# Performance work log

Measured on AMD Instinct MI355X. Metric: run time of the kernel, lower is better.

Reference implementation:

```python
import jax, jax.numpy as jnp
import numpy as np

N, DIM, H, D = 8192, 1152, 16, 72
SEGS = 4  # equal-length image segments


def setup_inputs() -> dict:
    key = jax.random.key(0)
    ks = jax.random.split(key, 8)
    s = 0.02
    return {
        "hidden_states": jax.random.normal(ks[0], (N, DIM), jnp.float32),
        "cos": jax.random.uniform(ks[1], (N, D), jnp.float32, -1.0, 1.0),
        "sin": jax.random.uniform(ks[2], (N, D), jnp.float32, -1.0, 1.0),
        "cu_seqlens": (jnp.arange(SEGS + 1, dtype=jnp.int32) * (N // SEGS)),
        "w_qkv": jax.random.normal(ks[3], (DIM, 3 * DIM), jnp.float32) * s,
        "b_qkv": jax.random.normal(ks[4], (3 * DIM,), jnp.float32) * s,
        "w_proj": jax.random.normal(ks[5], (DIM, DIM), jnp.float32) * s,
        "b_proj": jax.random.normal(ks[6], (DIM,), jnp.float32) * s,
    }


def _rope(x, cos, sin):
    # x: [N, H, D]; cos/sin: [N, 1, D]
    half = x.shape[-1] // 2
    x1, x2 = x[..., :half], x[..., half:]
    rot = jnp.concatenate([-x2, x1], axis=-1)
    return x * cos + rot * sin


def reference(hidden_states, cos, sin, cu_seqlens, w_qkv, b_qkv, w_proj, b_proj):
    n = hidden_states.shape[0]
    qkv = (hidden_states @ w_qkv + b_qkv).reshape(n, 3, H, D)
    q, k, v = qkv[:, 0], qkv[:, 1], qkv[:, 2]
    c = cos[:, None, :]
    s = sin[:, None, :]
    q = _rope(q, c, s)
    k = _rope(k, c, s)
    # equal-length segments derived statically from cu_seqlens
    segs = int(cu_seqlens.shape[0]) - 1
    L = n // segs
    qs = q.reshape(segs, L, H, D)
    ks = k.reshape(segs, L, H, D)
    vs = v.reshape(segs, L, H, D)
    scale = D ** -0.5
    scores = jnp.einsum("slhd,smhd->shlm", qs, ks) * scale
    attn = jax.nn.softmax(scores, axis=-1)
    out = jnp.einsum("shlm,smhd->slhd", attn, vs).reshape(n, DIM)
    return out @ w_proj + b_proj
```

## Files before the change

### kernel.cpp

```cpp
#include <hip/hip_runtime.h>
#include <hip/hip_bf16.h>
#include <cstdint>
#include <cstddef>

typedef __bf16 bf16;
typedef __attribute__((ext_vector_type(4))) __bf16 bf16x4;
typedef __attribute__((ext_vector_type(8))) __bf16 bf16x8;
typedef __attribute__((ext_vector_type(4))) float f32x4;
typedef __attribute__((ext_vector_type(16))) float f32x16;
typedef __attribute__((ext_vector_type(4))) float floatx4;
typedef __attribute__((ext_vector_type(2))) unsigned uint2_t;
typedef __attribute__((ext_vector_type(4))) unsigned uint4_t;

#define NTOK 8192
#define DIMM 1152
#define NH   16
#define HD   72
#define SEGS 4
#define SEGL 2048

__device__ __forceinline__ void gload16(const void* gsrc, void* ldst) {
  __builtin_amdgcn_global_load_lds(
      (const __attribute__((address_space(1))) void*)gsrc,
      (__attribute__((address_space(3))) void*)ldst,
      16, 0, 0);
}

__device__ __forceinline__ unsigned cvtpk(float a, float b) {
  unsigned r;
  asm volatile("v_cvt_pk_bf16_f32 %0, %1, %2" : "=v"(r) : "v"(a), "v"(b));
  return r;
}

__global__ __launch_bounds__(256) void k_prep(const float* __restrict__ hs,
                                              bf16* __restrict__ hsb,
                                              const float* __restrict__ wq,
                                              bf16* __restrict__ wqT,
                                              const float* __restrict__ wp,
                                              bf16* __restrict__ wpT) {
  __shared__ bf16 tile[64][73];
  const int b = blockIdx.x, t = threadIdx.x;
  if (b < 4608) {
    int i = b * 256 + t;
    const floatx4* s = (const floatx4*)hs + (size_t)i * 2;
    floatx4 a = s[0], c = s[1];
    uint4_t o;
    o[0] = cvtpk(a.x, a.y);
    o[1] = cvtpk(a.z, a.w);
    o[2] = cvtpk(c.x, c.y);
    o[3] = cvtpk(c.z, c.w);
    *((uint4_t*)hsb + i) = o;
    return;
  }
  const float* src; bf16* dst; int R, C, bx, by;
  if (b < 4608 + 1008) {
    int idx = b - 4608;
    src = wq; dst = wqT; R = 1152; C = 3456; bx = idx % 56; by = idx / 56;
  } else {
    int idx = b - 5616;
    src = wp; dst = wpT; R = 1152; C = 1152; bx = idx % 18; by = idx / 18;
  }
  int bc = bx * 64, br = by * 64;
#pragma unroll
  for (int i = 0; i < 16; i++) {
    int idx = i * 256 + t;
    int r = idx >> 6, c = idx & 63;
    float v = (bc + c < C) ? src[(size_t)(br + r) * C + bc + c] : 0.f;
    tile[c][r] = (bf16)v;
  }
  __syncthreads();
#pragma unroll
  for (int i = 0; i < 16; i++) {
    int idx = i * 256 + t;
    int r = idx >> 6, c = idx & 63;
    dst[(size_t)(bc + r) * R + br + c] = tile[r][c];
  }
}

template <int BM, int BN, int MI, int NI, int THREADS, bool OUT_F32, int MW>
__global__ __launch_bounds__(THREADS, MW) void k_gemmP(const bf16* __restrict__ A,
                                                       const bf16* __restrict__ Bt,
                                                       const float* __restrict__ bias,
                                                       void* __restrict__ Cout,
                                                       int M, int Nreal, int K, int gx) {
  __shared__ bf16 sA[3][BM * 32];
  __shared__ bf16 sB[3][BN * 32];
  constexpr int WN = BN / (NI * 16);
  constexpr int nA = (BM * 4) / THREADS;
  constexpr int nB = (BN * 4) / THREADS;
  constexpr int NLD = nA + nB;
  static_assert(NLD == 3 || NLD == 4 || NLD == 6, "vmcnt literal");
  const int t = threadIdx.x, wave = t >> 6, lane = t & 63;
  const int lr = lane & 15, lg = lane >> 4;
  const int nwg = gridDim.x, bid = blockIdx.x;
  const int swz = (bid & 7) * (nwg >> 3) + (bid >> 3);
  const int bx = swz % gx, by = swz / gx;
  const int m0 = by * BM, n0 = bx * BN;
  const int wr = wave / WN, wc = wave % WN;
  const int NS = K >> 5;

  f32x4 acc[MI][NI];
#pragma unroll
  for (int i = 0; i < MI; i++)
#pragma unroll
    for (int j = 0; j < NI; j++)
#pragma unroll
      for (int q = 0; q < 4; q++) acc[i][j][q] = 0.f;

  const bf16* Ab = A + (size_t)m0 * K;
  const bf16* Bb = Bt + (size_t)n0 * K;
  const int glsw = ((t & 3) ^ ((t >> 3) & 3)) * 8;
  const int rbase = t >> 2;

  auto STAGE = [&](int slot, int k0) {
#pragma unroll
    for (int p = 0; p < nA; ++p)
      gload16(Ab + (size_t)(rbase + p * (THREADS / 4)) * K + k0 + glsw,
              (char*)&sA[slot][0] + p * (THREADS * 16) + wave * 1024);
#pragma unroll
    for (int p = 0; p < nB; ++p)
      gload16(Bb + (size_t)(rbase + p * (THREADS / 4)) * K + k0 + glsw,
              (char*)&sB[slot][0] + p * (THREADS * 16) + wave * 1024);
  };

  const int swz4 = (lr >> 1) & 3;
  const int aoff = (wr * MI * 16 + lr) * 32 + ((lg ^ swz4) * 8);
  const int boff = (wc * NI * 16 + lr) * 32 + ((lg ^ swz4) * 8);

  STAGE(0, 0);
  STAGE(1, 32);

  int slot = 0;
  for (int j = 0; j < NS; ++j) {
    if (j == NS - 1) {
      asm volatile("s_waitcnt vmcnt(0)" ::: "memory");
    } else if constexpr (NLD == 3) {
      asm volatile("s_waitcnt vmcnt(3)" ::: "memory");
    } else if constexpr (NLD == 4) {
      asm volatile("s_waitcnt vmcnt(4)" ::: "memory");
    } else {
      asm volatile("s_waitcnt vmcnt(6)" ::: "memory");
    }
    __builtin_amdgcn_s_barrier();
    __builtin_amdgcn_sched_barrier(0);
    bf16x8 av[MI], bv[NI];
#pragma unroll
    for (int mi = 0; mi < MI; mi++)
      av[mi] = *(const bf16x8*)&sA[slot][aoff + mi * 512];
#pragma unroll
    for (int ni = 0; ni < NI; ni++)
      bv[ni] = *(const bf16x8*)&sB[slot][boff + ni * 512];
    asm volatile("s_waitcnt lgkmcnt(0)" ::: "memory");
    __builtin_amdgcn_sched_barrier(0);
    if (j + 2 < NS) {
      int s2 = slot + 2; if (s2 >= 3) s2 -= 3;
      STAGE(s2, (j + 2) * 32);
    }
    __builtin_amdgcn_s_setprio(1);
#pragma unroll
    for (int mi = 0; mi < MI; mi++)
#pragma unroll
      for (int ni = 0; ni < NI; ni++)
        acc[mi][ni] = __builtin_amdgcn_mfma_f32_16x16x32_bf16(av[mi], bv[ni], acc[mi][ni], 0, 0, 0);
    __builtin_amdgcn_s_setprio(0);
    if (++slot == 3) slot = 0;
  }

#pragma unroll
  for (int mi = 0; mi < MI; ++mi)
#pragma unroll
    for (int ni = 0; ni < NI; ++ni) {
      int col = n0 + wc * NI * 16 + ni * 16 + lr;
      if (col < Nreal) {
        float bc_ = bias[col];
#pragma unroll
        for (int j = 0; j < 4; j++) {
          int row = m0 + wr * MI * 16 + mi * 16 + lg * 4 + j;
          float v = acc[mi][ni][j] + bc_;
          if (OUT_F32)
            ((float*)Cout)[(size_t)row * Nreal + col] = v;
          else
            ((bf16*)Cout)[(size_t)row * Nreal + col] = (bf16)v;
        }
      }
    }
}

__global__ __launch_bounds__(256) void k_ropev(const bf16* __restrict__ qkv,
                                               const float* __restrict__ cs,
                                               const float* __restrict__ sn,
                                               bf16* __restrict__ Qp,
                                               bf16* __restrict__ Kp,
                                               bf16* __restrict__ Vt) {
  __shared__ bf16 tl[64][80];
  const int bid = blockIdx.x, t = threadIdx.x;
  if (bid < 2048) {
    const float QS = 0.17002323f;
    const int n0 = bid * 4;
#pragma unroll
    for (int it = 0; it < 6; ++it) {
      int idx = it * 256 + t;
      int tok = idx / 384;
      int r = idx - tok * 384;
      int which = r / 192;
      int r2 = r - which * 192;
      int h = r2 / 12;
      int d0 = (r2 - h * 12) * 8;
      int n = n0 + tok;
      bf16* dst = which ? Kp : Qp;
      size_t ob = ((((size_t)((n >> 11) * NH + h)) * 3 + (d0 >> 5)) * SEGL +
                   (n & 2047)) * 32 + (d0 & 31);
      if (d0 >= HD) {
        uint4_t z = {0u, 0u, 0u, 0u};
        *(uint4_t*)&dst[ob] = z;
        continue;
      }
      const bf16* rowp = qkv + (size_t)n * (3 * DIMM) + which * DIMM + h * HD;
      bf16x8 xv = *(const bf16x8*)&rowp[d0];
      float ov[8];
      if (d0 == 32) {
        bf16x4 a = *(const bf16x4*)&rowp[68];
        bf16x4 b = *(const bf16x4*)&rowp[0];
#pragma unroll
        for (int j = 0; j < 4; j++) { ov[j] = -(float)a[j]; ov[j + 4] = (float)b[j]; }
      } else if (d0 < 32) {
        bf16x4 a = *(const bf16x4*)&rowp[d0 + 36];
        bf16x4 b = *(const bf16x4*)&rowp[d0 + 40];
#pragma unroll
        for (int j = 0; j < 4; j++) { ov[j] = -(float)a[j]; ov[j + 4] = -(float)b[j]; }
      } else {
        bf16x4 a = *(const bf16x4*)&rowp[d0 - 36];
        bf16x4 b = *(const bf16x4*)&rowp[d0 - 32];
#pragma unroll
        for (int j = 0; j < 4; j++) { ov[j] = (float)a[j]; ov[j + 4] = (float)b[j]; }
      }
      const float* cr = cs + (size_t)n * HD + d0;
      const float* sr = sn + (size_t)n * HD + d0;
      floatx4 c0 = *(const floatx4*)cr, c1 = *(const floatx4*)(cr + 4);
      floatx4 s0 = *(const floatx4*)sr, s1 = *(const floatx4*)(sr + 4);
      float vv[8];
#pragma unroll
      for (int j = 0; j < 4; j++) {
        vv[j] = (float)xv[j] * c0[j] + ov[j] * s0[j];
        vv[j + 4] = (float)xv[j + 4] * c1[j] + ov[j + 4] * s1[j];
      }
      if (!which) {
#pragma unroll
        for (int j = 0; j < 8; j++) vv[j] *= QS;
      }
      uint4_t w;
      w[0] = cvtpk(vv[0], vv[1]);
      w[1] = cvtpk(vv[2], vv[3]);
      w[2] = cvtpk(vv[4], vv[5]);
      w[3] = cvtpk(vv[6], vv[7]);
      *(uint4_t*)&dst[ob] = w;
    }
  } else {
    int idx2 = bid - 2048;
    int s = idx2 >> 9, h = (idx2 >> 5) & 15, l0 = (idx2 & 31) * 64;
    for (int idx = t; idx < 64 * HD; idx += 256) {
      int l = idx / HD, d = idx - l * HD;
      tl[l][d] = qkv[(size_t)(s * SEGL + l0 + l) * (3 * DIMM) + 2 * DIMM + h * HD + d];
    }
    __syncthreads();
    for (int idx = t; idx < 96 * 64; idx += 256) {
      int d = idx >> 6, l = idx & 63;
      bf16 v = (d < HD) ? tl[l][d] : ((d == HD) ? (bf16)1.f : (bf16)0.f);
      Vt[((size_t)(s * NH + h) * 96 + d) * SEGL + l0 + l] = v;
    }
  }
}

__global__ __launch_bounds__(256, 2) void k_attn(const bf16* __restrict__ Qg,
                                                 const bf16* __restrict__ Kg,
                                                 const bf16* __restrict__ Vg,
                                                 bf16* __restrict__ Oo) {
  __shared__ bf16 sK[2][3 * 64 * 32];
  __shared__ bf16 sV[2][96 * 64];
  const int t = threadIdx.x, wave = t >> 6, lane = t & 63;
  const int c = lane & 31, hi = lane >> 5;
  const int bid = blockIdx.x;
  const int g = ((bid >> 6) << 3) | (bid & 7);
  const int qt = (bid >> 3) & 7;
  const int s = g >> 4, h = g & 15, q0 = qt * 256;
  const bf16* Qb = Qg + (size_t)(s * NH + h) * 3 * SEGL * 32;
  const bf16* Kb = Kg + (size_t)(s * NH + h) * 3 * SEGL * 32;
  const bf16* Vb = Vg + (size_t)(s * NH + h) * 96 * SEGL;

  const bf16* kq[3];
  const bf16* vq[3];
#pragma unroll
  for (int i = 0; i < 3; i++) {
    int ch = wave * 3 + i;
    int kk = ch >> 2;
    int r = (ch & 3) * 16 + (lane >> 2);
    int gg = (lane & 3) ^ ((r >> 1) & 3);
    kq[i] = Kb + (size_t)kk * (SEGL * 32) + (size_t)r * 32 + gg * 8;
    int rv = ch * 8 + (lane >> 3);
    int gv = (lane & 7) ^ (rv & 7);
    vq[i] = Vb + (size_t)rv * SEGL + gv * 8;
  }

  bf16x8 Qf[2][5];
#pragma unroll
  for (int sni = 0; sni < 2; sni++)
#pragma unroll
    for (int kk = 0; kk < 5; kk++) {
      int qr = q0 + wave * 64 + sni * 32 + c;
      Qf[sni][kk] = *(const bf16x8*)&Qb[(size_t)(kk >> 1) * (SEGL * 32) +
                                        (size_t)qr * 32 + ((kk & 1) * 2 + hi) * 8];
    }

#pragma unroll
  for (int i = 0; i < 3; i++) {
    gload16(kq[i], (char*)sK[0] + (wave * 3 + i) * 1024);
    gload16(vq[i], (char*)sV[0] + (wave * 3 + i) * 1024);
    kq[i] += 2048;
    vq[i] += 64;
  }
  __syncthreads();

  f32x16 accO[3][2];
#pragma unroll
  for (int df = 0; df < 3; df++)
#pragma unroll
    for (int sni = 0; sni < 2; sni++)
#pragma unroll
      for (int r = 0; r < 16; r++) accO[df][sni][r] = 0.f;
  f32x16 ZC;
#pragma unroll
  for (int r = 0; r < 16; r++) ZC[r] = 0.f;

  int cur = 0;
  for (int tile = 0; tile < 32; ++tile) {
    if (tile + 1 < 32) {
#pragma unroll
      for (int i = 0; i < 3; i++) {
        gload16(kq[i], (char*)sK[cur ^ 1] + (wave * 3 + i) * 1024);
        gload16(vq[i], (char*)sV[cur ^ 1] + (wave * 3 + i) * 1024);
        kq[i] += 2048;
        vq[i] += 64;
      }
    }

    f32x16 S[2][2];
    __builtin_amdgcn_s_setprio(1);
#pragma unroll
    for (int kk = 0; kk < 5; kk++) {
      bf16x8 Kf[2];
#pragma unroll
      for (int smi = 0; smi < 2; smi++) {
        int kr = smi * 32 + c;
        int gg = (((kk & 1) * 2 + hi) ^ ((kr >> 1) & 3));
        Kf[smi] = *(const bf16x8*)&sK[cur][(kk >> 1) * 2048 + kr * 32 + gg * 8];
      }
#pragma unroll
      for (int smi = 0; smi < 2; smi++)
#pragma unroll
        for (int sni = 0; sni < 2; sni++)
          S[smi][sni] = __builtin_amdgcn_mfma_f32_32x32x16_bf16(
              Kf[smi], Qf[sni][kk], kk ? S[smi][sni] : ZC, 0, 0, 0);
    }
    __builtin_amdgcn_s_setprio(0);

    __builtin_amdgcn_s_setprio(1);
#pragma unroll
    for (int kk = 0; kk < 4; kk++) {
      bf16x8 Vf[3];
#pragma unroll
      for (int df = 0; df < 3; df++) {
        int dr = df * 32 + c;
        int gg = ((kk * 2 + hi) ^ (dr & 7));
        Vf[df] = *(const bf16x8*)&sV[cur][dr * 64 + gg * 8];
      }
#pragma unroll
      for (int sni = 0; sni < 2; sni++) {
        const int smi = kk >> 1;
        const int base = (kk & 1) * 8;
        unsigned u0 = cvtpk(__builtin_amdgcn_exp2f(S[smi][sni][base + 0]),
                            __builtin_amdgcn_exp2f(S[smi][sni][base + 1]));
        unsigned u1 = cvtpk(__builtin_amdgcn_exp2f(S[smi][sni][base + 2]),
                            __builtin_amdgcn_exp2f(S[smi][sni][base + 3]));
        unsigned u2 = cvtpk(__builtin_amdgcn_exp2f(S[smi][sni][base + 4]),
                            __builtin_amdgcn_exp2f(S[smi][sni][base + 5]));
        unsigned u3 = cvtpk(__builtin_amdgcn_exp2f(S[smi][sni][base + 6]),
                            __builtin_amdgcn_exp2f(S[smi][sni][base + 7]));
        asm volatile("v_permlane32_swap_b32 %0, %1" : "+v"(u0), "+v"(u2));
        asm volatile("v_permlane32_swap_b32 %0, %1" : "+v"(u1), "+v"(u3));
        union { bf16x8 v; unsigned u[4]; } pb;
        pb.u[0] = u0; pb.u[1] = u1; pb.u[2] = u2; pb.u[3] = u3;
#pragma unroll
        for (int df = 0; df < 3; df++)
          accO[df][sni] = __builtin_amdgcn_mfma_f32_32x32x16_bf16(Vf[df], pb.v, accO[df][sni], 0, 0, 0);
      }
    }
    __builtin_amdgcn_s_setprio(0);

    __syncthreads();
    cur ^= 1;
  }

#pragma unroll
  for (int sni = 0; sni < 2; sni++) {
    float lown = accO[2][sni][4];
    float lv = lown + __shfl_xor(lown, 32, 64);
    float inv = 1.f / lv;
    int token = s * SEGL + q0 + wave * 64 + sni * 32 + c;
#pragma unroll
    for (int df = 0; df < 3; df++)
#pragma unroll
      for (int rg = 0; rg < 4; rg++) {
        int d0 = df * 32 + rg * 8 + hi * 4;
        if (d0 < HD) {
          uint2_t w;
          w[0] = cvtpk(accO[df][sni][rg * 4 + 0] * inv, accO[df][sni][rg * 4 + 1] * inv);
          w[1] = cvtpk(accO[df][sni][rg * 4 + 2] * inv, accO[df][sni][rg * 4 + 3] * inv);
          *(uint2_t*)&Oo[(size_t)token * DIMM + h * HD + d0] = w;
        }
      }
  }
}

extern "C" void kernel_launch(void* const* d_in, const int* in_sizes, int n_in,
                              void* d_out, int out_size, void* d_ws, size_t ws_size,
                              hipStream_t stream) {
  (void)in_sizes; (void)n_in; (void)out_size; (void)ws_size;
  const float* hs     = (const float*)d_in[0];
  const float* cosp   = (const float*)d_in[1];
  const float* sinp   = (const float*)d_in[2];
  const float* w_qkv  = (const float*)d_in[4];
  const float* b_qkv  = (const float*)d_in[5];
  const float* w_proj = (const float*)d_in[6];
  const float* b_proj = (const float*)d_in[7];
  float* out = (float*)d_out;

  char* ws = (char*)d_ws;
  bf16* hsb    = (bf16*)(ws + 0);
  bf16* wprojT = (bf16*)(ws + 26836992);
  bf16* qkv    = (bf16*)(ws + 29491200);
  bf16* Qp     = (bf16*)(ws + 86114304);
  bf16* Kp     = (bf16*)(ws + 111280128);
  bf16* Vt     = (bf16*)(ws + 136445952);
  bf16* ao     = (bf16*)(ws + 161611776);
  bf16* wqkvT  = (bf16*)(ws + 161611776);

  k_prep<<<5940, 256, 0, stream>>>(hs, hsb, w_qkv, wqkvT, w_proj, wprojT);
  k_gemmP<256, 128, 8, 4, 256, false, 2><<<896, 256, 0, stream>>>(
      hsb, wqkvT, b_qkv, (void*)qkv, 8192, 3456, 1152, 28);
  k_ropev<<<4096, 256, 0, stream>>>(qkv, cosp, sinp, Qp, Kp, Vt);
  k_attn<<<512, 256, 0, stream>>>(Qp, Kp, Vt, ao);
  k_gemmP<128, 128, 4, 4, 256, true, 3><<<576, 256, 0, stream>>>(
      ao, wprojT, b_proj, (void*)out, 8192, 1152, 1152, 9);
}
```

Before: 252.6 us.

## Use 256x256-tile 8-wave QKV GEMM with phased LDS double buffering

Replaces the 256x128 QKV projection GEMM with a new 512-thread kernel that computes 256x256 output tiles using BK=64. Each k-step is split into four phases that interleave per-half global-to-LDS loads with MFMA work, with explicit vmcnt waits, barriers and setprio. The larger tile is meant to raise operand reuse and cut global traffic per FLOP. In exchange it uses more registers and LDS per workgroup, and a 3456-wide N leaves a padded last tile (13.5 tiles), so some compute is wasted.

Result: no change. 249.5 us (-1.2%).

```diff
diff --git a/kernel.cpp b/kernel.cpp
--- a/kernel.cpp
+++ b/kernel.cpp
@@ -75,6 +75,119 @@
     int r = idx >> 6, c = idx & 63;
     dst[(size_t)(bc + r) * R + br + c] = tile[r][c];
   }
+}
+
+#define QPHASE(D, CH, KK, READB, STG, VM)                                      \
+  {                                                                            \
+    asm volatile("s_waitcnt vmcnt(" VM ")" ::: "memory");                      \
+    __builtin_amdgcn_s_barrier();                                              \
+    __builtin_amdgcn_sched_barrier(0);                                         \
+    bf16x8 av[4];                                                              \
+    _Pragma("unroll")                                                          \
+    for (int mi = 0; mi < 4; mi++)                                             \
+      av[mi] = *(const bf16x8*)&sA[D][wr][(CH * 64 + mi * 16 + lr) * 64 + ga[KK]]; \
+    if (READB) {                                                               \
+      _Pragma("unroll")                                                        \
+      for (int ni = 0; ni < 4; ni++)                                           \
+        bv[ni] = *(const bf16x8*)&sB[D][bh][(bro + ni * 16 + lr) * 64 + ga[KK]]; \
+    }                                                                          \
+    asm volatile("s_waitcnt lgkmcnt(0)" ::: "memory");                         \
+    __builtin_amdgcn_sched_barrier(0);                                         \
+    STG;                                                                       \
+    __builtin_amdgcn_s_setprio(1);                                             \
+    _Pragma("unroll")                                                          \
+    for (int mi = 0; mi < 4; mi++)                                             \
+      _Pragma("unroll")                                                        \
+      for (int ni = 0; ni < 4; ni++)                                           \
+        acc[CH * 4 + mi][ni] = __builtin_amdgcn_mfma_f32_16x16x32_bf16(        \
+            av[mi], bv[ni], acc[CH * 4 + mi][ni], 0, 0, 0);                    \
+    __builtin_amdgcn_s_setprio(0);                                             \
+  }
+
+__global__ __launch_bounds__(512, 2) void k_gemm8p(const bf16* __restrict__ A,
+                                                   const bf16* __restrict__ Bt,
+                                                   const float* __restrict__ bias,
+                                                   bf16* __restrict__ Cout,
+                                                   int M, int Nreal, int K, int gx) {
+  __shared__ bf16 sA[2][2][128 * 64];
+  __shared__ bf16 sB[2][2][128 * 64];
+  const int t = threadIdx.x, wave = t >> 6, lane = t & 63;
+  const int lr = lane & 15, lg = lane >> 4;
+  const int nwg = gridDim.x, bid = blockIdx.x;
+  const int swz = (bid & 7) * (nwg >> 3) + (bid >> 3);
+  const int bx = swz % gx, by = swz / gx;
+  const int m0 = by * 256, n0 = bx * 256;
+  const int wr = wave >> 2, wc = wave & 3;
+  const int bh = wc >> 1, bro = (wc & 1) * 64;
+  const int NS = K >> 6;
+
+  f32x4 acc[8][4];
+#pragma unroll
+  for (int i = 0; i < 8; i++)
+#pragma unroll
+    for (int j = 0; j < 4; j++)
+#pragma unroll
+      for (int q = 0; q < 4; q++) acc[i][j][q] = 0.f;
+
+  const bf16* Ab = A + (size_t)m0 * K;
+  const bf16* Bb = Bt + (size_t)n0 * K;
+  const int glsw8 = (((t & 7) ^ ((t >> 3) & 7)) * 8);
+  const bf16* Asrc[2][2];
+  const bf16* Bsrc[2][2];
+#pragma unroll
+  for (int h = 0; h < 2; h++)
+#pragma unroll
+    for (int p = 0; p < 2; p++) {
+      Asrc[h][p] = Ab + (size_t)(h * 128 + p * 64 + (t >> 3)) * K + glsw8;
+      Bsrc[h][p] = Bb + (size_t)(h * 128 + p * 64 + (t >> 3)) * K + glsw8;
+    }
+  auto STA = [&](int d2, int h, int ttt) {
+    gload16(Asrc[h][0] + (size_t)ttt * 64, (char*)&sA[d2][h][0] + t * 16);
+    gload16(Asrc[h][1] + (size_t)ttt * 64, (char*)&sA[d2][h][0] + 8192 + t * 16);
+  };
+  auto STB = [&](int d2, int h, int ttt) {
+    gload16(Bsrc[h][0] + (size_t)ttt * 64, (char*)&sB[d2][h][0] + t * 16);
+    gload16(Bsrc[h][1] + (size_t)ttt * 64, (char*)&sB[d2][h][0] + 8192 + t * 16);
+  };
+  const int ga[2] = { ((0 + lg) ^ (lr & 7)) * 8, ((4 + lg) ^ (lr & 7)) * 8 };
+
+  STB(0, 0, 0);
+  STB(0, 1, 0);
+  STA(0, 0, 0);
+  STA(0, 1, 0);
+  STB(1, 0, 1);
+
+  bf16x8 bv[4];
+  int tt = 0;
+  for (; tt < NS - 1; ++tt) {
+    const int d = tt & 1, dn = d ^ 1;
+    QPHASE(d, 0, 0, true,  { STB(dn, 1, tt + 1); }, "4");
+    QPHASE(d, 1, 0, false, { STA(dn, 0, tt + 1); }, "4");
+    QPHASE(d, 0, 1, true,  { STA(dn, 1, tt + 1); }, "6");
+    QPHASE(d, 1, 1, false, { if (tt + 2 < NS) STB(d, 0, tt + 2); }, "6");
+  }
+  {
+    const int d = tt & 1;
+    QPHASE(d, 0, 0, true,  {;}, "0");
+    QPHASE(d, 1, 0, false, {;}, "0");
+    QPHASE(d, 0, 1, true,  {;}, "0");
+    QPHASE(d, 1, 1, false, {;}, "0");
+  }
+
+#pragma unroll
+  for (int mi = 0; mi < 8; ++mi)
+#pragma unroll
+    for (int ni = 0; ni < 4; ++ni) {
+      int col = n0 + wc * 64 + ni * 16 + lr;
+      if (col < Nreal) {
+        float bc_ = bias[col];
+#pragma unroll
+        for (int j = 0; j < 4; j++) {
+          int row = m0 + wr * 128 + mi * 16 + lg * 4 + j;
+          Cout[(size_t)row * Nreal + col] = (bf16)(acc[mi][ni][j] + bc_);
+        }
+      }
+    }
 }
 
 template <int BM, int BN, int MI, int NI, int THREADS, bool OUT_F32, int MW>
@@ -445,8 +558,7 @@
   bf16* wqkvT  = (bf16*)(ws + 161611776);
 
   k_prep<<<5940, 256, 0, stream>>>(hs, hsb, w_qkv, wqkvT, w_proj, wprojT);
-  k_gemmP<256, 128, 8, 4, 256, false, 2><<<896, 256, 0, stream>>>(
-      hsb, wqkvT, b_qkv, (void*)qkv, 8192, 3456, 1152, 28);
+  k_gemm8p<<<448, 512, 0, stream>>>(hsb, wqkvT, b_qkv, qkv, 8192, 3456, 1152, 14);
   k_ropev<<<4096, 256, 0, stream>>>(qkv, cosp, sinp, Qp, Kp, Vt);
   k_attn<<<512, 256, 0, stream>>>(Qp, Kp, Vt, ao);
   k_gemmP<128, 128, 4, 4, 256, true, 3><<<576, 256, 0, stream>>>(
```
